# Kernel optimization log

Measured on AMD Instinct MI355X. Metric: run time of the kernel, lower is better.

The kernel has to match this reference:

```python
import jax, jax.numpy as jnp
import numpy as np

VOCAB, XS, HS, NCLASS = 32000, 256, 256, 2
B, DEPTH = 128, 9
NTREE = 2 ** (DEPTH + 1) - 1  # 1023 nodes per perfect binary tree


def setup_inputs() -> dict:
    key = jax.random.key(0)
    ks = jax.random.split(key, 10)
    return {
        'types1': jax.random.randint(ks[0], (B, NTREE), 0, VOCAB, dtype=jnp.int32),
        'types2': jax.random.randint(ks[1], (B, NTREE), 0, VOCAB, dtype=jnp.int32),
        'emb': jax.random.normal(ks[2], (VOCAB, XS), jnp.float32) * 0.1,
        'W_iou': jax.random.normal(ks[3], (3 * HS, XS), jnp.float32) * 0.05,
        'U_iou': jax.random.normal(ks[4], (3 * HS, HS), jnp.float32) * 0.05,
        'b_iou': jnp.zeros((1, 3 * HS), jnp.float32),
        'U_f_w': jax.random.normal(ks[5], (HS, HS), jnp.float32) * 0.05,
        'U_f_b': jnp.zeros((HS,), jnp.float32),
        'cls_w': jax.random.normal(ks[6], (NCLASS, HS), jnp.float32) * 0.05,
        'cls_b': jnp.zeros((NCLASS,), jnp.float32),
    }


def _tree_forward(types, emb, W_iou, U_iou, b_iou, U_f_w, U_f_b):
    # types: [B, NTREE] heap layout (node j has children 2j+1, 2j+2)
    x = emb[types]                       # [B, N, XS] embedding gather
    wx = x @ W_iou.T                     # [B, N, 3H] leaf iou (DGL reduce overwrites it for internal nodes)
    h = jnp.zeros((types.shape[0], NTREE, HS), wx.dtype)
    c = jnp.zeros_like(h)
    for lvl in range(DEPTH, -1, -1):     # bottom-up topological levels (static)
        idx = np.arange(2 ** lvl - 1, 2 ** (lvl + 1) - 1)
        if lvl == DEPTH:  # leaves: no mailbox, keep W_iou(x)
            iou = wx[:, idx] + b_iou
            c_sum = 0.0
        else:
            ch = np.stack([2 * idx + 1, 2 * idx + 2], axis=-1)  # [n, 2]
            h_ch = h[:, ch]              # [B, n, 2, H] child mailbox
            c_ch = c[:, ch]
            h_tild = h_ch.sum(axis=2)
            f = jax.nn.sigmoid(h_ch @ U_f_w.T + U_f_b)
            c_sum = (f * c_ch).sum(axis=2)
            iou = h_tild @ U_iou.T + b_iou  # overwrites wx per DGL semantics
        i, o, u = jnp.split(iou, 3, axis=-1)
        c_new = jax.nn.sigmoid(i) * jnp.tanh(u) + c_sum
        h_new = jax.nn.sigmoid(o) * jnp.tanh(c_new)
        h = h.at[:, idx].set(h_new)
        c = c.at[:, idx].set(c_new)
    return h.mean(axis=1)                # AvgPooling over nodes -> [B, H]


def reference(types1, types2, emb, W_iou, U_iou, b_iou, U_f_w, U_f_b, cls_w, cls_b):
    rep1 = _tree_forward(types1, emb, W_iou, U_iou, b_iou, U_f_w, U_f_b)
    rep2 = _tree_forward(types2, emb, W_iou, U_iou, b_iou, U_f_w, U_f_b)
    return jnp.abs(rep1 - rep2) @ cls_w.T + cls_b  # [B, NCLASS]
```

## Files before the change

### kernel.cpp

```cpp
#include <hip/hip_runtime.h>
#include <math.h>


typedef _Float16 h16;
typedef h16 f16x8 __attribute__((ext_vector_type(8)));
typedef float f32x4 __attribute__((ext_vector_type(4)));

#define HS 256
#define NTREE 1023
#define B2 256

#define DMA16(gp, lp) __builtin_amdgcn_global_load_lds( \
    (const __attribute__((address_space(1))) void*)(gp), \
    (__attribute__((address_space(3))) void*)(lp), 16, 0, 0)

__device__ __forceinline__ float sigf(float x){
  return __builtin_amdgcn_rcpf(1.0f + exp2f(x * -1.44269504f));
}
__device__ __forceinline__ float tanh_fast(float x){
  return 2.0f*__builtin_amdgcn_rcpf(1.0f + exp2f(x * -2.88539008f)) - 1.0f;
}
__device__ __forceinline__ float sig_mul_tanh(float a, float b){
  const float E1 = exp2f(a * -1.44269504f);
  const float E2 = exp2f(fminf(b * -2.88539008f, 126.0f));
  return (1.0f - E2) * __builtin_amdgcn_rcpf((1.0f + E1) * (1.0f + E2));
}

__global__ __launch_bounds__(256) void convert_all(const float* __restrict__ emb,
    const float* __restrict__ Ufw, const float* __restrict__ Uiou,
    const float* __restrict__ Wiou, h16* __restrict__ emb16,
    h16* __restrict__ W16, h16* __restrict__ Wx16, float* __restrict__ rep){
  if (blockIdx.x < 64)
    ((float4*)rep)[blockIdx.x*256 + threadIdx.x] = make_float4(0.f,0.f,0.f,0.f);
  const size_t i0 = ((size_t)blockIdx.x*256 + threadIdx.x)*8;
  const float* src; h16* dst; size_t off;
  if (i0 < 8192000UL){ src = emb;  dst = emb16;       off = i0; }
  else if (i0 < 8257536UL){ src = Ufw;  dst = W16;        off = i0 - 8192000UL; }
  else if (i0 < 8454144UL){ src = Uiou; dst = W16+65536;  off = i0 - 8257536UL; }
  else               { src = Wiou; dst = Wx16;       off = i0 - 8454144UL; }
  const float4 v0 = *(const float4*)&src[off];
  const float4 v1 = *(const float4*)&src[off+4];
  f16x8 o;
  o[0]=(h16)v0.x; o[1]=(h16)v0.y; o[2]=(h16)v0.z; o[3]=(h16)v0.w;
  o[4]=(h16)v1.x; o[5]=(h16)v1.y; o[6]=(h16)v1.z; o[7]=(h16)v1.w;
  *(f16x8*)&dst[off] = o;
}

__global__ __launch_bounds__(256) void swizzle_w(const h16* __restrict__ W16,
    h16* __restrict__ Wfrag){
  const int tid = blockIdx.x*256 + threadIdx.x;
  const int lane = tid & 63;
  const int f    = (tid >> 6) & 15;
  const int kc   = (tid >> 10) & 7;
  const int cb   = tid >> 13;
  const int g = f >> 2, cf = f & 3;
  const int row = g*256 + cb*64 + cf*16 + (lane & 15);
  const int col = kc*32 + (lane >> 4)*8;
  const f16x8 v = *(const f16x8*)&W16[(size_t)row*256 + col];
  *(f16x8*)&Wfrag[(size_t)tid*8] = v;
}

__global__ __launch_bounds__(256) void wxv_mfma(const h16* __restrict__ emb16,
    const h16* __restrict__ Wx16, h16* __restrict__ WxV){
  __shared__ h16 As[64*40];
  __shared__ h16 Bs[64*40];
  const int t = threadIdx.x, lane = t & 63, wave = t >> 6;
  const int q = lane >> 4, li = lane & 15;
  const int waveR = wave & 1, waveC = wave >> 1;
  const int bm = blockIdx.x*64, bn = blockIdx.y*64;
  const size_t aAddr = ((size_t)(bm + (t>>2)))*256 + (t&3)*8;
  const size_t bAddr = ((size_t)(bn + (t>>2)))*256 + (t&3)*8;
  const int ldsOff = (t>>2)*40 + (t&3)*8;
  f32x4 acc[2][2] = {};
  for (int k0 = 0; k0 < 256; k0 += 32){
    const f16x8 a = *(const f16x8*)&emb16[aAddr + k0];
    const f16x8 b = *(const f16x8*)&Wx16[bAddr + k0];
    __syncthreads();
    *(f16x8*)&As[ldsOff] = a;
    *(f16x8*)&Bs[ldsOff] = b;
    __syncthreads();
    #pragma unroll
    for (int rt=0; rt<2; ++rt){
      const f16x8 av = *(const f16x8*)&As[(waveR*32 + rt*16 + li)*40 + q*8];
      #pragma unroll
      for (int ct=0; ct<2; ++ct){
        const f16x8 bv = *(const f16x8*)&Bs[(waveC*32 + ct*16 + li)*40 + q*8];
        acc[rt][ct] = __builtin_amdgcn_mfma_f32_16x16x32_f16(av, bv, acc[rt][ct], 0,0,0);
      }
    }
  }
  #pragma unroll
  for (int rt=0; rt<2; ++rt)
    #pragma unroll
    for (int ct=0; ct<2; ++ct){
      const int col = bn + waveC*32 + ct*16 + li;
      #pragma unroll
      for (int reg=0; reg<4; ++reg){
        const int row = bm + waveR*32 + rt*16 + q*4 + reg;
        WxV[(size_t)row*768 + col] = (h16)acc[rt][ct][reg];
      }
    }
}

__global__ __launch_bounds__(256) void leaf_kernel(const int* __restrict__ t1,
    const int* __restrict__ t2, const h16* __restrict__ WxV,
    const float* __restrict__ biou, h16* __restrict__ leafH,
    h16* __restrict__ leafC, float* __restrict__ rep){
  const int r = blockIdx.y, jg = blockIdx.x, k = threadIdx.x;
  const int* tp = (r < 128) ? t1 : t2;
  const int b = r & 127;
  const float bi = biou[k], bo = biou[256+k], bu = biou[512+k];
  float s = 0.f;
  for (int jj=0; jj<64; ++jj){
    const int leafIdx = jg*64 + jj;
    const size_t v = (size_t)tp[b*NTREE + 511 + leafIdx];
    const float vi = (float)WxV[v*768 + k] + bi;
    const float vo = (float)WxV[v*768 + 256 + k] + bo;
    const float vu = (float)WxV[v*768 + 512 + k] + bu;
    const float c = sigf(vi) * tanh_fast(vu);
    const float h = sigf(vo) * tanh_fast(c);
    const size_t o = ((size_t)r*512 + leafIdx)*HS + k;
    leafH[o] = (h16)h;
    leafC[o] = (h16)c;
    s += h;
  }
  atomicAdd(&rep[r*HS + k], s);
}

__global__ __launch_bounds__(256,3) void level_mfma(
    const h16* __restrict__ hChild, const h16* __restrict__ cChild,
    const h16* __restrict__ Wfrag,
    const float* __restrict__ biou, const float* __restrict__ Ufb,
    h16* __restrict__ hUpW, h16* __restrict__ cPar,
    int log2n, int leafLvl, int cbN, int cOff, int ndOff){
  const int n = 1 << log2n;
  const int mask2 = 2*n - 1;
  __shared__ h16 ldsA[4*8*64*8];
  __shared__ h16 ldsB[16*64*8];
  const int t = threadIdx.x, w = t >> 6, l = t & 63;
  const int q = l >> 4, li = l & 15;
  const int waveR = w & 1, waveC = w >> 1;
  const int bx = blockIdx.x;

  {
    const int grow = bx*64 + w*16 + li;
    size_t abase;
    if (leafLvl){
      abase = (size_t)grow * 256;
    } else {
      const int cidx = grow & mask2;
      const int rr   = grow >> (log2n + 1);
      abase = ((size_t)(cOff + cidx)*256 + rr)*256;
    }
    #pragma unroll
    for (int kc=0; kc<8; ++kc)
      DMA16(hChild + abase + kc*32 + q*8, &ldsA[(w*8 + kc)*512]);
  }

  for (int cb=0; cb<cbN; ++cb){
    const int cbi = blockIdx.y*cbN + cb;
    const int colBase = cbi*64;
    const h16* wfBase = Wfrag + (size_t)cbi*8*16*512 + (size_t)l*8;

    #pragma unroll
    for (int i=0; i<4; ++i)
      DMA16(wfBase + ((size_t)(w*4 + i))*512, &ldsB[(w*4 + i)*512]);
    __syncthreads();

    f32x4 acc[4][2][2] = {};
    #pragma unroll
    for (int kc=0; kc<8; ++kc){
      f16x8 aF[2], bF[4][2];
      #pragma unroll
      for (int rt=0; rt<2; ++rt)
        aF[rt] = *(const f16x8*)&ldsA[(((waveR*2 + rt)*8 + kc)*64 + l)*8];
      #pragma unroll
      for (int g=0; g<4; ++g)
        #pragma unroll
        for (int ct=0; ct<2; ++ct)
          bF[g][ct] = *(const f16x8*)&ldsB[((g*4 + waveC*2 + ct)*64 + l)*8];
      __syncthreads();
      if (kc < 7){
        #pragma unroll
        for (int i=0; i<4; ++i)
          DMA16(wfBase + ((size_t)(kc+1)*16 + w*4 + i)*512,
                &ldsB[(w*4 + i)*512]);
      }
      #pragma unroll
      for (int g=0; g<4; ++g)
        #pragma unroll
        for (int rt=0; rt<2; ++rt)
          #pragma unroll
          for (int ct=0; ct<2; ++ct)
            acc[g][rt][ct] = __builtin_amdgcn_mfma_f32_16x16x32_f16(
                aF[rt], bF[g][ct], acc[g][rt][ct], 0,0,0);
      __syncthreads();
    }

    #pragma unroll
    for (int ct=0; ct<2; ++ct){
      const int c = colBase + waveC*32 + ct*16 + li;
      const float fb  = Ufb[c];
      const float bi_ = biou[c], bo_ = biou[256+c], bu_ = biou[512+c];
      #pragma unroll
      for (int rt=0; rt<2; ++rt){
        #pragma unroll
        for (int pp=0; pp<2; ++pp){
          const int crel = waveR*32 + rt*16 + q*4 + 2*pp;
          const int m = bx*32 + (crel >> 1);
          const int rr2 = m >> log2n;
          const int jn = m & (n - 1);
          const float cl = (float)cChild[(size_t)(bx*64 + crel)*256 + c];
          const float cr = (float)cChild[(size_t)(bx*64 + crel + 1)*256 + c];
          const float fl = sigf(acc[0][rt][ct][2*pp]   + fb);
          const float fr = sigf(acc[0][rt][ct][2*pp+1] + fb);
          const float iv = acc[1][rt][ct][2*pp] + acc[1][rt][ct][2*pp+1] + bi_;
          const float ov = acc[2][rt][ct][2*pp] + acc[2][rt][ct][2*pp+1] + bo_;
          const float uv = acc[3][rt][ct][2*pp] + acc[3][rt][ct][2*pp+1] + bu_;
          const float cnew = sig_mul_tanh(iv, uv) + fl*cl + fr*cr;
          const float hnew = sig_mul_tanh(ov, cnew);
          hUpW[(((size_t)(ndOff + jn))*256 + rr2)*256 + c] = (h16)hnew;
          cPar[((size_t)m)*256 + c] = (h16)cnew;
        }
      }
    }
  }
}

__global__ __launch_bounds__(256) void rep_accum(const h16* __restrict__ H,
    float* __restrict__ rep, int nrows, int chunk){
  const int r = blockIdx.y, k = threadIdx.x;
  const int n0 = blockIdx.x * chunk;
  int n1 = n0 + chunk; if (n1 > nrows) n1 = nrows;
  float s = 0.f;
  for (int nd = n0; nd < n1; ++nd)
    s += (float)H[((size_t)nd*256 + r)*HS + k];
  atomicAdd(&rep[r*HS + k], s);
}

__global__ __launch_bounds__(256) void cls_kernel(const float* __restrict__ rep,
    const float* __restrict__ clsw, const float* __restrict__ clsb,
    float* __restrict__ out){
  const int b = blockIdx.x, k = threadIdx.x;
  const float d = fabsf(rep[b*HS + k] - rep[(128+b)*HS + k]) * (1.0f/1023.0f);
  __shared__ float r0[256], r1[256];
  r0[k] = d * clsw[k];
  r1[k] = d * clsw[HS + k];
  __syncthreads();
  for (int off = 128; off > 0; off >>= 1){
    if (k < off){ r0[k] += r0[k+off]; r1[k] += r1[k+off]; }
    __syncthreads();
  }
  if (k == 0){
    out[b*2 + 0] = r0[0] + clsb[0];
    out[b*2 + 1] = r1[0] + clsb[1];
  }
}

extern "C" void kernel_launch(void* const* d_in, const int* in_sizes, int n_in,
                              void* d_out, int out_size, void* d_ws, size_t ws_size,
                              hipStream_t stream){
  const int*   types1 = (const int*)d_in[0];
  const int*   types2 = (const int*)d_in[1];
  const float* emb    = (const float*)d_in[2];
  const float* Wiou   = (const float*)d_in[3];
  const float* Uiou   = (const float*)d_in[4];
  const float* biou   = (const float*)d_in[5];
  const float* Ufw    = (const float*)d_in[6];
  const float* Ufb    = (const float*)d_in[7];
  const float* clsw   = (const float*)d_in[8];
  const float* clsb   = (const float*)d_in[9];
  float* out = (float*)d_out;

  h16* ws      = (h16*)d_ws;
  h16* leafH   = ws;
  h16* leafC   = ws + 33554432UL;
  h16* WxV     = ws + 67108864UL;
  h16* cA      = ws + 91684864UL;
  h16* cB      = ws + 108462080UL;
  h16* emb16   = cB;
  h16* Wx16    = cB + 8192000UL;
  float* rep   = (float*)(ws + 116850688UL);
  h16* Wfrag   = ws + 116981760UL;
  h16* W16     = ws;
  h16* hUpLow  = leafC;
  h16* hUpHigh = WxV;

  convert_all<<<4224, 256, 0, stream>>>(emb, Ufw, Uiou, Wiou, emb16, W16, Wx16, rep);
  swizzle_w<<<256, 256, 0, stream>>>(W16, Wfrag);
  wxv_mfma<<<dim3(500,12), 256, 0, stream>>>(emb16, Wx16, WxV);
  leaf_kernel<<<dim3(8, B2), 256, 0, stream>>>(types1, types2, WxV, biou,
                                               leafH, leafC, rep);

  const h16* cprev = nullptr;
  for (int lvl = 8; lvl >= 0; --lvl){
    const int children = 512 << lvl;
    const int cbN = (lvl >= 6) ? 4 : 1;
    h16* cout = ((8 - lvl) & 1) ? cB : cA;
    const h16* cin = (lvl == 8) ? leafC : cprev;
    const h16* hin = (lvl == 8) ? leafH : ((lvl == 7) ? hUpHigh : hUpLow);
    h16* hUpW      = (lvl == 8) ? hUpHigh : hUpLow;
    const int cOff  = (lvl == 7) ? 0 : ((1 << (lvl + 1)) - 1);
    const int ndOff = (lvl == 8) ? 0 : ((1 << lvl) - 1);
    level_mfma<<<dim3(children/64, 4/cbN), 256, 0, stream>>>(
        hin, cin, Wfrag, biou, Ufb, hUpW, cout,
        lvl, (lvl == 8) ? 1 : 0, cbN, cOff, ndOff);
    cprev = cout;
  }
  rep_accum<<<dim3(2, B2), 256, 0, stream>>>(hUpLow,  rep, 255, 128);
  rep_accum<<<dim3(2, B2), 256, 0, stream>>>(hUpHigh, rep, 256, 128);
  cls_kernel<<<128, 256, 0, stream>>>(rep, clsw, clsb, out);
}
```

Measured before the change: 514.9 us.

## Precompute per-vocab leaf states and child gate products to skip leaf-level GEMM

Result: slower. 534.1 us (+3.7%).

```diff
diff --git a/kernel.cpp b/kernel.cpp
--- a/kernel.cpp
+++ b/kernel.cpp
@@ -16,9 +16,6 @@
 
 __device__ __forceinline__ float sigf(float x){
   return __builtin_amdgcn_rcpf(1.0f + exp2f(x * -1.44269504f));
-}
-__device__ __forceinline__ float tanh_fast(float x){
-  return 2.0f*__builtin_amdgcn_rcpf(1.0f + exp2f(x * -2.88539008f)) - 1.0f;
 }
 __device__ __forceinline__ float sig_mul_tanh(float a, float b){
   const float E1 = exp2f(a * -1.44269504f);
@@ -102,29 +99,111 @@
     }
 }
 
-__global__ __launch_bounds__(256) void leaf_kernel(const int* __restrict__ t1,
-    const int* __restrict__ t2, const h16* __restrict__ WxV,
-    const float* __restrict__ biou, h16* __restrict__ leafH,
-    h16* __restrict__ leafC, float* __restrict__ rep){
+__global__ __launch_bounds__(256) void gt_mfma(const h16* __restrict__ hT,
+    const h16* __restrict__ W16, float* __restrict__ GT){
+  __shared__ h16 As[64*40];
+  __shared__ h16 Bs[64*40];
+  const int t = threadIdx.x, lane = t & 63, wave = t >> 6;
+  const int q = lane >> 4, li = lane & 15;
+  const int waveR = wave & 1, waveC = wave >> 1;
+  const int bm = blockIdx.x*64, bn = blockIdx.y*64;
+  const size_t aAddr = ((size_t)(bm + (t>>2)))*256 + (t&3)*8;
+  const size_t bAddr = ((size_t)(bn + (t>>2)))*256 + (t&3)*8;
+  const int ldsOff = (t>>2)*40 + (t&3)*8;
+  f32x4 acc[2][2] = {};
+  for (int k0 = 0; k0 < 256; k0 += 32){
+    const f16x8 a = *(const f16x8*)&hT[aAddr + k0];
+    const f16x8 b = *(const f16x8*)&W16[bAddr + k0];
+    __syncthreads();
+    *(f16x8*)&As[ldsOff] = a;
+    *(f16x8*)&Bs[ldsOff] = b;
+    __syncthreads();
+    #pragma unroll
+    for (int rt=0; rt<2; ++rt){
+      const f16x8 av = *(const f16x8*)&As[(waveR*32 + rt*16 + li)*40 + q*8];
+      #pragma unroll
+      for (int ct=0; ct<2; ++ct){
+        const f16x8 bv = *(const f16x8*)&Bs[(waveC*32 + ct*16 + li)*40 + q*8];
+        acc[rt][ct] = __builtin_amdgcn_mfma_f32_16x16x32_f16(av, bv, acc[rt][ct], 0,0,0);
+      }
+    }
+  }
+  #pragma unroll
+  for (int rt=0; rt<2; ++rt)
+    #pragma unroll
+    for (int ct=0; ct<2; ++ct){
+      const int col = bn + waveC*32 + ct*16 + li;
+      #pragma unroll
+      for (int reg=0; reg<4; ++reg){
+        const int row = bm + waveR*32 + rt*16 + q*4 + reg;
+        GT[(size_t)row*1024 + col] = acc[rt][ct][reg];
+      }
+    }
+}
+
+__global__ __launch_bounds__(256) void type_cell(const h16* __restrict__ WxV,
+    const float* __restrict__ biou, h16* __restrict__ hT, h16* __restrict__ cT){
+  const int tid = blockIdx.x*256 + threadIdx.x;
+  const int row = tid >> 5;
+  const int k8  = (tid & 31) * 8;
+  const f16x8 vi8 = *(const f16x8*)&WxV[(size_t)row*768 + k8];
+  const f16x8 vo8 = *(const f16x8*)&WxV[(size_t)row*768 + 256 + k8];
+  const f16x8 vu8 = *(const f16x8*)&WxV[(size_t)row*768 + 512 + k8];
+  f16x8 hO, cO;
+  #pragma unroll
+  for (int j=0; j<8; ++j){
+    const float vi = (float)vi8[j] + biou[k8+j];
+    const float vo = (float)vo8[j] + biou[256+k8+j];
+    const float vu = (float)vu8[j] + biou[512+k8+j];
+    const float c = sig_mul_tanh(vi, vu);
+    const float h = sig_mul_tanh(vo, c);
+    cO[j] = (h16)c; hO[j] = (h16)h;
+  }
+  *(f16x8*)&hT[(size_t)row*256 + k8] = hO;
+  *(f16x8*)&cT[(size_t)row*256 + k8] = cO;
+}
+
+__global__ __launch_bounds__(256) void leaf_rep(const int* __restrict__ t1,
+    const int* __restrict__ t2, const h16* __restrict__ hT,
+    float* __restrict__ rep){
   const int r = blockIdx.y, jg = blockIdx.x, k = threadIdx.x;
   const int* tp = (r < 128) ? t1 : t2;
   const int b = r & 127;
-  const float bi = biou[k], bo = biou[256+k], bu = biou[512+k];
   float s = 0.f;
   for (int jj=0; jj<64; ++jj){
-    const int leafIdx = jg*64 + jj;
-    const size_t v = (size_t)tp[b*NTREE + 511 + leafIdx];
-    const float vi = (float)WxV[v*768 + k] + bi;
-    const float vo = (float)WxV[v*768 + 256 + k] + bo;
-    const float vu = (float)WxV[v*768 + 512 + k] + bu;
-    const float c = sigf(vi) * tanh_fast(vu);
-    const float h = sigf(vo) * tanh_fast(c);
-    const size_t o = ((size_t)r*512 + leafIdx)*HS + k;
-    leafH[o] = (h16)h;
-    leafC[o] = (h16)c;
-    s += h;
+    const int v = tp[b*NTREE + 511 + jg*64 + jj];
+    s += (float)hT[(size_t)v*256 + k];
   }
   atomicAdd(&rep[r*HS + k], s);
+}
+
+__global__ __launch_bounds__(256) void lvl8_cell(const int* __restrict__ t1,
+    const int* __restrict__ t2, const float* __restrict__ GT,
+    const h16* __restrict__ cT, const float* __restrict__ biou,
+    const float* __restrict__ Ufb, h16* __restrict__ hUpHigh,
+    h16* __restrict__ cPar){
+  const int k = threadIdx.x;
+  const float fb = Ufb[k];
+  const float bi = biou[k], bo = biou[256+k], bu = biou[512+k];
+  const int m0 = blockIdx.x*32;
+  for (int p=0; p<32; ++p){
+    const int m = m0 + p, rr = m >> 8, jn = m & 255;
+    const int* tp = (rr < 128) ? t1 : t2;
+    const int b = rr & 127;
+    const size_t vl = (size_t)tp[b*NTREE + 511 + 2*jn];
+    const size_t vr = (size_t)tp[b*NTREE + 512 + 2*jn];
+    const float fl = sigf(GT[vl*1024 + k] + fb);
+    const float fr = sigf(GT[vr*1024 + k] + fb);
+    const float iv = GT[vl*1024 + 256 + k] + GT[vr*1024 + 256 + k] + bi;
+    const float ov = GT[vl*1024 + 512 + k] + GT[vr*1024 + 512 + k] + bo;
+    const float uv = GT[vl*1024 + 768 + k] + GT[vr*1024 + 768 + k] + bu;
+    const float cl = (float)cT[vl*256 + k];
+    const float cr = (float)cT[vr*256 + k];
+    const float cnew = sig_mul_tanh(iv, uv) + fl*cl + fr*cr;
+    const float hnew = sig_mul_tanh(ov, cnew);
+    hUpHigh[((size_t)jn*256 + rr)*256 + k] = (h16)hnew;
+    cPar[(size_t)m*256 + k] = (h16)cnew;
+  }
 }
 
 __global__ __launch_bounds__(256,3) void level_mfma(
@@ -132,7 +211,7 @@
     const h16* __restrict__ Wfrag,
     const float* __restrict__ biou, const float* __restrict__ Ufb,
     h16* __restrict__ hUpW, h16* __restrict__ cPar,
-    int log2n, int leafLvl, int cbN, int cOff, int ndOff){
+    int log2n, int cbN, int cOff, int ndOff){
   const int n = 1 << log2n;
   const int mask2 = 2*n - 1;
   __shared__ h16 ldsA[4*8*64*8];
@@ -144,14 +223,9 @@
 
   {
     const int grow = bx*64 + w*16 + li;
-    size_t abase;
-    if (leafLvl){
-      abase = (size_t)grow * 256;
-    } else {
-      const int cidx = grow & mask2;
-      const int rr   = grow >> (log2n + 1);
-      abase = ((size_t)(cOff + cidx)*256 + rr)*256;
-    }
+    const int cidx = grow & mask2;
+    const int rr   = grow >> (log2n + 1);
+    const size_t abase = ((size_t)(cOff + cidx)*256 + rr)*256;
     #pragma unroll
     for (int kc=0; kc<8; ++kc)
       DMA16(hChild + abase + kc*32 + q*8, &ldsA[(w*8 + kc)*512]);
@@ -273,38 +347,40 @@
   float* out = (float*)d_out;
 
   h16* ws      = (h16*)d_ws;
-  h16* leafH   = ws;
-  h16* leafC   = ws + 33554432UL;
-  h16* WxV     = ws + 67108864UL;
-  h16* cA      = ws + 91684864UL;
-  h16* cB      = ws + 108462080UL;
-  h16* emb16   = cB;
-  h16* Wx16    = cB + 8192000UL;
-  float* rep   = (float*)(ws + 116850688UL);
-  h16* Wfrag   = ws + 116981760UL;
-  h16* W16     = ws;
-  h16* hUpLow  = leafC;
-  h16* hUpHigh = WxV;
+  float* GT    = (float*)ws;
+  h16* WxV     = ws;
+  h16* emb16   = ws + 24576000UL;
+  h16* Wx16    = ws + 32768000UL;
+  h16* hUpLow  = ws;
+  h16* cB      = ws + 16711680UL;
+  h16* hT      = ws + 65536000UL;
+  h16* cT      = ws + 73728000UL;
+  h16* hUpHigh = ws + 81920000UL;
+  h16* cA      = ws + 98697216UL;
+  h16* W16     = ws + 115474432UL;
+  h16* Wfrag   = ws + 115736576UL;
+  float* rep   = (float*)(ws + 116260864UL);
 
   convert_all<<<4224, 256, 0, stream>>>(emb, Ufw, Uiou, Wiou, emb16, W16, Wx16, rep);
   swizzle_w<<<256, 256, 0, stream>>>(W16, Wfrag);
   wxv_mfma<<<dim3(500,12), 256, 0, stream>>>(emb16, Wx16, WxV);
-  leaf_kernel<<<dim3(8, B2), 256, 0, stream>>>(types1, types2, WxV, biou,
-                                               leafH, leafC, rep);
-
-  const h16* cprev = nullptr;
-  for (int lvl = 8; lvl >= 0; --lvl){
+  type_cell<<<4000, 256, 0, stream>>>(WxV, biou, hT, cT);
+  gt_mfma<<<dim3(500,16), 256, 0, stream>>>(hT, W16, GT);
+  leaf_rep<<<dim3(8, B2), 256, 0, stream>>>(types1, types2, hT, rep);
+  lvl8_cell<<<2048, 256, 0, stream>>>(types1, types2, GT, cT, biou, Ufb,
+                                      hUpHigh, cA);
+
+  const h16* cprev = cA;
+  for (int lvl = 7; lvl >= 0; --lvl){
     const int children = 512 << lvl;
     const int cbN = (lvl >= 6) ? 4 : 1;
     h16* cout = ((8 - lvl) & 1) ? cB : cA;
-    const h16* cin = (lvl == 8) ? leafC : cprev;
-    const h16* hin = (lvl == 8) ? leafH : ((lvl == 7) ? hUpHigh : hUpLow);
-    h16* hUpW      = (lvl == 8) ? hUpHigh : hUpLow;
+    const h16* hin = (lvl == 7) ? hUpHigh : hUpLow;
     const int cOff  = (lvl == 7) ? 0 : ((1 << (lvl + 1)) - 1);
-    const int ndOff = (lvl == 8) ? 0 : ((1 << lvl) - 1);
+    const int ndOff = (1 << lvl) - 1;
     level_mfma<<<dim3(children/64, 4/cbN), 256, 0, stream>>>(
-        hin, cin, Wfrag, biou, Ufb, hUpW, cout,
-        lvl, (lvl == 8) ? 1 : 0, cbN, cOff, ndOff);
+        hin, cprev, Wfrag, biou, Ufb, hUpLow, cout,
+        lvl, cbN, cOff, ndOff);
     cprev = cout;
   }
   rep_accum<<<dim3(2, B2), 256, 0, stream>>>(hUpLow,  rep, 255, 128);
```
